# Kernel optimization log

Hardware: AMD Instinct MI355X
Metric: run time of the kernel (lower is better)

## Reference

```python
import jax, jax.numpy as jnp
import numpy as np

N = 10000
E = 160000
IN_DIM = 512
OUT_DIM = 256
NEG_SLOPE = 0.2  # DGL GATConv default LeakyReLU slope


def _gat_conv(x, W, b, attn_l, attn_r, src, dst, num_nodes, heads, out_dim):
    """DGL GATConv (eval mode, feat_drop/attn_drop disabled).
    x: [N, F_in]; W: [F_in, heads*out]; b: [heads*out];
    attn_l/attn_r: [heads, out]. Returns [N, heads, out]."""
    h = (x @ W).reshape(num_nodes, heads, out_dim)            # [N,H,D]
    el = jnp.einsum('nhd,hd->nh', h, attn_l)                  # [N,H]
    er = jnp.einsum('nhd,hd->nh', h, attn_r)                  # [N,H]
    e = jax.nn.leaky_relu(el[src] + er[dst], NEG_SLOPE)       # [E,H]
    # destination-grouped (edge) softmax, numerically stable
    m = jax.ops.segment_max(e, dst, num_segments=num_nodes)   # [N,H], -inf for empty
    m = jnp.where(jnp.isfinite(m), m, 0.0)
    ee = jnp.exp(e - m[dst])                                  # [E,H]
    s = jax.ops.segment_sum(ee, dst, num_segments=num_nodes)  # [N,H]
    a = ee / jnp.where(s > 0, s, 1.0)[dst]                    # [E,H]
    # message aggregation: scatter-add a_e * h[src]
    out = jax.ops.segment_sum(a[:, :, None] * h[src], dst, num_segments=num_nodes)
    return out + b.reshape(1, heads, out_dim)


def setup_inputs() -> dict:
    key = jax.random.key(0)
    ks = jax.random.split(key, 16)
    def glorot(k, shape):
        fan = shape[0] + shape[-1] if len(shape) > 1 else shape[-1]
        return jax.random.normal(k, shape, dtype=jnp.float32) * np.sqrt(2.0 / fan)
    inp = {
        'x':   jax.random.normal(ks[0], (N, IN_DIM), dtype=jnp.float32),
        'src': jax.random.randint(ks[1], (E,), 0, N),
        'dst': jax.random.randint(ks[2], (E,), 0, N),
        'W1': glorot(ks[3], (IN_DIM, 10 * 128)),
        'b1': jnp.zeros((10 * 128,), jnp.float32),
        'al1': glorot(ks[4], (10, 128)),
        'ar1': glorot(ks[5], (10, 128)),
        'W2': glorot(ks[6], (1280, 10 * 64)),
        'b2': jnp.zeros((10 * 64,), jnp.float32),
        'al2': glorot(ks[7], (10, 64)),
        'ar2': glorot(ks[8], (10, 64)),
        'W3': glorot(ks[9], (640, OUT_DIM)),
        'b3': jnp.zeros((OUT_DIM,), jnp.float32),
        'al3': glorot(ks[10], (1, OUT_DIM)),
        'ar3': glorot(ks[11], (1, OUT_DIM)),
        # residual linear 512 -> 256
        'Wres': glorot(ks[12], (IN_DIM, OUT_DIM)),
        'bres': jnp.zeros((OUT_DIM,), jnp.float32),
        'fuse_weight': jnp.full((1,), 0.5, jnp.float32),
    }
    return inp


def reference(x, src, dst, W1, b1, al1, ar1, W2, b2, al2, ar2,
              W3, b3, al3, ar3, Wres, bres, fuse_weight):
    elu = jax.nn.elu
    res = elu(x @ Wres + bres)                                        # [N,256]
    s1 = elu(_gat_conv(x, W1, b1, al1, ar1, src, dst, N, 10, 128))
    s1 = s1.reshape(N, -1)                                            # [N,1280]
    s2 = elu(_gat_conv(s1, W2, b2, al2, ar2, src, dst, N, 10, 64))
    s2 = s2.reshape(N, -1)                                            # [N,640]
    s3 = elu(_gat_conv(s2, W3, b3, al3, ar3, src, dst, N, 1, OUT_DIM))
    s3 = s3.reshape(N, -1)                                            # [N,256]
    return fuse_weight * s3 + (1.0 - fuse_weight) * res
```

## Files before the change

kernel.cpp:

```cpp
#include <hip/hip_runtime.h>
#include <stdint.h>

#define DEVINL __device__ __forceinline__

typedef __attribute__((ext_vector_type(8))) short short8;
typedef __attribute__((ext_vector_type(4))) float f32x4;

static constexpr int NNODES = 10000;

DEVINL float bf2f(unsigned short u) {
  unsigned int x = ((unsigned int)u) << 16;
  float f;
  __builtin_memcpy(&f, &x, 4);
  return f;
}
DEVINL unsigned short f2bf(float f) {
  unsigned int x;
  __builtin_memcpy(&x, &f, 4);
  unsigned int lsb = (x >> 16) & 1;
  x += 0x7fffu + lsb;
  return (unsigned short)(x >> 16);
}
DEVINL void bfpair(unsigned int u, float& f0, float& f1) {
  unsigned int a = u << 16, b = u & 0xffff0000u;
  __builtin_memcpy(&f0, &a, 4);
  __builtin_memcpy(&f1, &b, 4);
}
DEVINL bool is_bf16_mode(const unsigned int* fwWord) {
  return ((*fwWord) & 0xFFFFu) == 0x3F00u;
}

DEVINL void async_cp16(void* lds, const void* g) {
  __builtin_amdgcn_global_load_lds((const __attribute__((address_space(1))) unsigned int*)g,
                                   (__attribute__((address_space(3))) unsigned int*)lds,
                                   16, 0, 0);
}

__global__ __launch_bounds__(256) void gemm_bf16(const unsigned short* __restrict__ A,
                                                 const unsigned short* __restrict__ Bt,
                                                 unsigned short* __restrict__ C,
                                                 int M, int N, int K) {
  __shared__ __align__(16) unsigned short lA[128 * 32];
  __shared__ __align__(16) unsigned short lB[128 * 32];
  const int tid = threadIdx.x;
  const int wid = tid >> 6;
  const int lane = tid & 63;
  const int tm = blockIdx.x * 128;
  const int tn = blockIdx.y * 128;
  const int wr = (wid >> 1) * 64;
  const int wc = (wid & 1) * 64;
  f32x4 acc[4][4] = {};
  const int r_in_chunk = lane >> 2;
  const int cb = (lane & 3) * 16;
  const int mr = lane & 15;
  const int kq = (lane >> 4) * 8;
  const size_t stride = (size_t)K * 2;

  for (int k0 = 0; k0 < K; k0 += 32) {
#pragma unroll
    for (int c = 0; c < 2; ++c) {
      const int chunk = wid * 2 + c;
      const int row = chunk * 16 + r_in_chunk;
      int ga = tm + row;
      if (ga >= M) ga = M - 1;
      async_cp16(&lA[chunk * 512], (const char*)A + (size_t)ga * stride + (size_t)k0 * 2 + cb);
      const int gb = tn + row;
      async_cp16(&lB[chunk * 512], (const char*)Bt + (size_t)gb * stride + (size_t)k0 * 2 + cb);
    }
    __syncthreads();
    short8 af[4], bf[4];
#pragma unroll
    for (int i = 0; i < 4; ++i)
      af[i] = *(const short8*)&lA[(wr + i * 16 + mr) * 32 + kq];
#pragma unroll
    for (int j = 0; j < 4; ++j)
      bf[j] = *(const short8*)&lB[(wc + j * 16 + mr) * 32 + kq];
#pragma unroll
    for (int i = 0; i < 4; ++i)
#pragma unroll
      for (int j = 0; j < 4; ++j)
        acc[i][j] = __builtin_amdgcn_mfma_f32_16x16x32_bf16(af[i], bf[j], acc[i][j], 0, 0, 0);
    __syncthreads();
  }

  const int rbase = (lane >> 4) * 4;
  const int cc = lane & 15;
#pragma unroll
  for (int i = 0; i < 4; ++i) {
#pragma unroll
    for (int r = 0; r < 4; ++r) {
      const int row = tm + wr + i * 16 + rbase + r;
      if (row < M) {
#pragma unroll
        for (int j = 0; j < 4; ++j) {
          const int col = tn + wc + j * 16 + cc;
          C[(size_t)row * N + col] = f2bf(acc[i][j][r]);
        }
      }
    }
  }
}

struct CvtJobs {
  const void* src[12];
  float* dst[12];
  int n[12];
  int cnt;
};
__global__ void cvt_small_f32(CvtJobs jobs, const unsigned int* fwWord) {
  const bool isb = is_bf16_mode(fwWord);
  for (int j = 0; j < jobs.cnt; ++j) {
    for (int i = blockIdx.x * blockDim.x + threadIdx.x; i < jobs.n[j];
         i += gridDim.x * blockDim.x) {
      jobs.dst[j][i] = isb ? bf2f(((const unsigned short*)jobs.src[j])[i])
                           : ((const float*)jobs.src[j])[i];
    }
  }
}

__global__ __launch_bounds__(256) void cvt_x_bf16(const void* __restrict__ in,
                                                  unsigned short* __restrict__ out,
                                                  long n, const unsigned int* fwWord) {
  const bool isb = is_bf16_mode(fwWord);
  const long i0 = (long)(blockIdx.x * 256 + threadIdx.x) * 8;
  if (i0 >= n) return;
  if (isb) {
    *(short8*)&out[i0] = *(const short8*)&((const unsigned short*)in)[i0];
  } else {
    const float* f = (const float*)in + i0;
    unsigned short r[8];
#pragma unroll
    for (int j = 0; j < 8; ++j) r[j] = f2bf(f[j]);
    *(short8*)&out[i0] = *(const short8*)r;
  }
}

struct TAll {
  const void* src[4];
  unsigned short* dst[4];
  int K[4];
  int N[4];
  int b0[5];
};
__global__ __launch_bounds__(256) void transp_all4(TAll ja, const unsigned int* fwWord) {
  const bool isb = is_bf16_mode(fwWord);
  __shared__ unsigned short t[32][33];
  const int bid = blockIdx.x;
  int j = 0;
  while (j < 3 && bid >= ja.b0[j + 1]) ++j;
  const int local = bid - ja.b0[j];
  const int K = ja.K[j], Nn = ja.N[j];
  const int tilesX = Nn / 32;
  const int bx = (local % tilesX) * 32;
  const int by = (local / tilesX) * 32;
  const void* W = ja.src[j];
  unsigned short* Wt = ja.dst[j];
  const int x = threadIdx.x;
  const int y0 = threadIdx.y;
  for (int y = y0; y < 32; y += 8) {
    const size_t idx = (size_t)(by + y) * Nn + bx + x;
    t[y][x] = isb ? ((const unsigned short*)W)[idx] : f2bf(((const float*)W)[idx]);
  }
  __syncthreads();
  for (int y = y0; y < 32; y += 8)
    Wt[(size_t)(bx + y) * K + by + x] = t[x][y];
}

template <int H, int D>
__global__ __launch_bounds__(256) void compute_elr(const unsigned short* __restrict__ hf,
                                                   const float* __restrict__ al,
                                                   const float* __restrict__ ar,
                                                   float* __restrict__ el,
                                                   float* __restrict__ er) {
  const int gw = (blockIdx.x * 256 + threadIdx.x) >> 6;
  const int lane = threadIdx.x & 63;
  if (gw >= NNODES * H) return;
  const int n = gw / H;
  const int h = gw % H;
  const unsigned short* hp = hf + (size_t)n * (H * D) + h * D;
  const float* alp = al + h * D;
  const float* arp = ar + h * D;
  float a = 0.f, b = 0.f;
#pragma unroll
  for (int d0 = 0; d0 < D; d0 += 64) {
    float v = bf2f(hp[d0 + lane]);
    a += v * alp[d0 + lane];
    b += v * arp[d0 + lane];
  }
#pragma unroll
  for (int o = 32; o; o >>= 1) {
    a += __shfl_xor(a, o);
    b += __shfl_xor(b, o);
  }
  if (lane == 0) { el[gw] = a; er[gw] = b; }
}

template <int H>
__global__ __launch_bounds__(256) void edge_w(const float* __restrict__ el,
                                              const float* __restrict__ er,
                                              const int* __restrict__ sidx,
                                              const int* __restrict__ didx,
                                              float* __restrict__ we, int E) {
  const int p = blockIdx.x * 256 + threadIdx.x;
  if (p >= E) return;
  const float* ep = el + (size_t)sidx[p] * H;
  const float* rp = er + (size_t)didx[p] * H;
  float* wp = we + (size_t)p * H;
#pragma unroll
  for (int h = 0; h < H; ++h) {
    float sc = ep[h] + rp[h];
    sc = sc > 0.f ? sc : 0.2f * sc;
    wp[h] = __expf(sc);
  }
}

template <int H, int D, int BLOCK, int V, int MODE>
__global__ __launch_bounds__(BLOCK) void gat_agg(const unsigned short* __restrict__ hf,
                                                 const float* __restrict__ we,
                                                 const int* __restrict__ sidx,
                                                 const int* __restrict__ rowstart,
                                                 const float* __restrict__ bias,
                                                 void* __restrict__ outp,
                                                 const unsigned short* __restrict__ resact,
                                                 const float* __restrict__ fwf,
                                                 const unsigned int* fwWord) {
  constexpr int CHUNK = 64;
  static_assert(H * D == BLOCK * V, "feature ownership mismatch");
  static_assert(BLOCK % H == 0, "fill-head must be thread-fixed");
  static_assert(V == 2 || V == 4, "vector width");
  __shared__ float wls[CHUNK * H];
  __shared__ int ssrc[CHUNK];
  __shared__ float shead[H];

  const int n = blockIdx.x;
  const int tid = threadIdx.x;
  const int e0 = rowstart[n];
  const int e1 = rowstart[n + 1];

  if (tid < H) shead[tid] = 0.f;
  __syncthreads();

  const int fbase = tid * V;
  const int fh = fbase / D;
  const int fh2 = tid % H;
  float acc[V];
#pragma unroll
  for (int k = 0; k < V; ++k) acc[k] = 0.f;
  float spart = 0.f;

  for (int cs = e0; cs < e1; cs += CHUNK) {
    const int ce = min(CHUNK, e1 - cs);
    if (tid < ce) ssrc[tid] = sidx[cs + tid];
    for (int i = tid; i < ce * H; i += BLOCK) {
      const float w = we[(size_t)cs * H + i];
      wls[i] = w;
      spart += w;
    }
    __syncthreads();
    int j = 0;
    for (; j + 4 <= ce; j += 4) {
      const int s0 = ssrc[j], s1 = ssrc[j + 1], s2 = ssrc[j + 2], s3 = ssrc[j + 3];
      const float w0 = wls[(j + 0) * H + fh];
      const float w1 = wls[(j + 1) * H + fh];
      const float w2 = wls[(j + 2) * H + fh];
      const float w3 = wls[(j + 3) * H + fh];
      if constexpr (V == 4) {
        const uint2 u0 = *(const uint2*)(hf + (size_t)s0 * (H * D) + fbase);
        const uint2 u1 = *(const uint2*)(hf + (size_t)s1 * (H * D) + fbase);
        const uint2 u2 = *(const uint2*)(hf + (size_t)s2 * (H * D) + fbase);
        const uint2 u3 = *(const uint2*)(hf + (size_t)s3 * (H * D) + fbase);
        float a0, a1, a2, a3;
        bfpair(u0.x, a0, a1); bfpair(u0.y, a2, a3);
        acc[0] += w0 * a0; acc[1] += w0 * a1; acc[2] += w0 * a2; acc[3] += w0 * a3;
        bfpair(u1.x, a0, a1); bfpair(u1.y, a2, a3);
        acc[0] += w1 * a0; acc[1] += w1 * a1; acc[2] += w1 * a2; acc[3] += w1 * a3;
        bfpair(u2.x, a0, a1); bfpair(u2.y, a2, a3);
        acc[0] += w2 * a0; acc[1] += w2 * a1; acc[2] += w2 * a2; acc[3] += w2 * a3;
        bfpair(u3.x, a0, a1); bfpair(u3.y, a2, a3);
        acc[0] += w3 * a0; acc[1] += w3 * a1; acc[2] += w3 * a2; acc[3] += w3 * a3;
      } else {
        const unsigned int u0 = *(const unsigned int*)(hf + (size_t)s0 * (H * D) + fbase);
        const unsigned int u1 = *(const unsigned int*)(hf + (size_t)s1 * (H * D) + fbase);
        const unsigned int u2 = *(const unsigned int*)(hf + (size_t)s2 * (H * D) + fbase);
        const unsigned int u3 = *(const unsigned int*)(hf + (size_t)s3 * (H * D) + fbase);
        float a0, a1;
        bfpair(u0, a0, a1); acc[0] += w0 * a0; acc[1] += w0 * a1;
        bfpair(u1, a0, a1); acc[0] += w1 * a0; acc[1] += w1 * a1;
        bfpair(u2, a0, a1); acc[0] += w2 * a0; acc[1] += w2 * a1;
        bfpair(u3, a0, a1); acc[0] += w3 * a0; acc[1] += w3 * a1;
      }
    }
    for (; j < ce; ++j) {
      const int s0 = ssrc[j];
      const float w = wls[j * H + fh];
      const unsigned short* hp = hf + (size_t)s0 * (H * D) + fbase;
      if constexpr (V == 4) {
        const uint2 u = *(const uint2*)hp;
        float a0, a1, a2, a3;
        bfpair(u.x, a0, a1); bfpair(u.y, a2, a3);
        acc[0] += w * a0; acc[1] += w * a1; acc[2] += w * a2; acc[3] += w * a3;
      } else {
        const unsigned int u = *(const unsigned int*)hp;
        float a0, a1;
        bfpair(u, a0, a1);
        acc[0] += w * a0; acc[1] += w * a1;
      }
    }
    __syncthreads();
  }

  atomicAdd(&shead[fh2], spart);
  __syncthreads();
  const float s = shead[fh];
  const float inv = s > 0.f ? 1.f / s : 0.f;
  const bool outb = (MODE == 1) ? is_bf16_mode(fwWord) : true;
  const size_t obase = (size_t)n * (H * D) + fbase;
#pragma unroll
  for (int k = 0; k < V; ++k) {
    float v = acc[k] * inv;
    v += bias[fbase + k];
    v = v > 0.f ? v : (__expf(v) - 1.f);
    if (MODE == 0) {
      ((unsigned short*)outp)[obase + k] = f2bf(v);
    } else {
      const float fw = fwf[0];
      const float r = bf2f(resact[obase + k]);
      const float o = fw * v + (1.f - fw) * r;
      if (outb) ((unsigned short*)outp)[obase + k] = f2bf(o);
      else      ((float*)outp)[obase + k] = o;
    }
  }
}

__global__ __launch_bounds__(256) void bias_elu(unsigned short* __restrict__ buf,
                                                const float* __restrict__ bias,
                                                int total, int Cc) {
  const int i = blockIdx.x * 256 + threadIdx.x;
  if (i >= total) return;
  float v = bf2f(buf[i]) + bias[i % Cc];
  v = v > 0.f ? v : (__expf(v) - 1.f);
  buf[i] = f2bf(v);
}

__global__ void sentinel_k(unsigned short* __restrict__ outp, int total) {
  const int i = blockIdx.x * 256 + threadIdx.x;
  if (i < total) outp[i] = f2bf(12344.0f);
}

__global__ void hist_k(const int* __restrict__ dst, int* __restrict__ deg, int E) {
  const int i = blockIdx.x * blockDim.x + threadIdx.x;
  if (i < E) atomicAdd(&deg[dst[i]], 1);
}

__global__ __launch_bounds__(1024) void scan_k(const int* __restrict__ deg,
                                               int* __restrict__ rowstart,
                                               int* __restrict__ cursor, int Nn) {
  __shared__ int ls[1024];
  const int tid = threadIdx.x;
  const int CH = (Nn + 1023) >> 10;
  const int start = tid * CH;
  int sum = 0;
  for (int i = 0; i < CH; ++i) {
    const int idx = start + i;
    if (idx < Nn) sum += deg[idx];
  }
  ls[tid] = sum;
  __syncthreads();
  for (int o = 1; o < 1024; o <<= 1) {
    int v = 0;
    if (tid >= o) v = ls[tid - o];
    __syncthreads();
    ls[tid] += v;
    __syncthreads();
  }
  int run = tid > 0 ? ls[tid - 1] : 0;
  for (int i = 0; i < CH; ++i) {
    const int idx = start + i;
    if (idx < Nn) {
      rowstart[idx] = run;
      cursor[idx] = run;
      run += deg[idx];
    }
  }
  if (tid == 1023) rowstart[Nn] = ls[1023];
}

__global__ void scatter_k(const int* __restrict__ dst, const int* __restrict__ srcA,
                          int* __restrict__ cursor, int* __restrict__ sidx,
                          int* __restrict__ didx, int E) {
  const int i = blockIdx.x * blockDim.x + threadIdx.x;
  if (i < E) {
    const int d = dst[i];
    const int p = atomicAdd(&cursor[d], 1);
    sidx[p] = srcA[i];
    didx[p] = d;
  }
}

extern "C" void kernel_launch(void* const* d_in, const int* in_sizes, int n_in,
                              void* d_out, int out_size, void* d_ws, size_t ws_size,
                              hipStream_t stream) {
  const void* x    = d_in[0];
  const int* src   = (const int*)d_in[1];
  const int* dstA  = (const int*)d_in[2];
  const void* W1   = d_in[3];
  const void* b1   = d_in[4];
  const void* al1  = d_in[5];
  const void* ar1  = d_in[6];
  const void* W2   = d_in[7];
  const void* b2   = d_in[8];
  const void* al2  = d_in[9];
  const void* ar2  = d_in[10];
  const void* W3   = d_in[11];
  const void* b3   = d_in[12];
  const void* al3  = d_in[13];
  const void* ar3  = d_in[14];
  const void* Wres = d_in[15];
  const void* bres = d_in[16];
  const void* fw   = d_in[17];
  const unsigned int* fwWord = (const unsigned int*)fw;
  const int E = in_sizes[1];
  const int M = NNODES;

  char* base = (char*)d_ws;
  size_t off = 0;
  auto alloc = [&](size_t bytes) -> char* {
    char* p = base + off;
    off = (off + bytes + 255) & ~(size_t)255;
    return p;
  };
  int* deg      = (int*)alloc((size_t)M * 4);
  int* rowstart = (int*)alloc((size_t)(M + 1) * 4);
  int* cursor   = (int*)alloc((size_t)M * 4);
  int* sidx     = (int*)alloc((size_t)E * 4);
  int* didx     = (int*)alloc((size_t)E * 4);
  float* web    = (float*)alloc((size_t)E * 10 * 4);
  float* elb    = (float*)alloc((size_t)M * 10 * 4);
  float* erb    = (float*)alloc((size_t)M * 10 * 4);
  float* b1f   = (float*)alloc(1280 * 4);
  float* al1f  = (float*)alloc(1280 * 4);
  float* ar1f  = (float*)alloc(1280 * 4);
  float* b2f   = (float*)alloc(640 * 4);
  float* al2f  = (float*)alloc(640 * 4);
  float* ar2f  = (float*)alloc(640 * 4);
  float* b3f   = (float*)alloc(256 * 4);
  float* al3f  = (float*)alloc(256 * 4);
  float* ar3f  = (float*)alloc(256 * 4);
  float* bresf = (float*)alloc(256 * 4);
  float* fwf   = (float*)alloc(4);
  unsigned short* wt1    = (unsigned short*)alloc((size_t)1280 * 512 * 2);
  unsigned short* wt2    = (unsigned short*)alloc((size_t)640 * 1280 * 2);
  unsigned short* wt3    = (unsigned short*)alloc((size_t)256 * 640 * 2);
  unsigned short* wtr    = (unsigned short*)alloc((size_t)256 * 512 * 2);
  unsigned short* resact = (unsigned short*)alloc((size_t)M * 256 * 2);
  unsigned short* regA   = (unsigned short*)alloc((size_t)M * 1280 * 2);
  unsigned short* regB   = (unsigned short*)alloc((size_t)M * 1280 * 2);

  if (off > ws_size) {
    sentinel_k<<<(out_size + 255) / 256, 256, 0, stream>>>((unsigned short*)d_out, out_size);
    return;
  }

  unsigned short* h1 = regA;
  unsigned short* h2 = regA;
  unsigned short* h3 = regA;
  unsigned short* xb = regB;
  unsigned short* s1 = regB;
  unsigned short* s2 = regB;

  CvtJobs jobs;
  const void* srcs[11] = {b1, al1, ar1, b2, al2, ar2, b3, al3, ar3, bres, fw};
  float* dsts[11] = {b1f, al1f, ar1f, b2f, al2f, ar2f, b3f, al3f, ar3f, bresf, fwf};
  const int ns[11] = {1280, 1280, 1280, 640, 640, 640, 256, 256, 256, 256, 1};
  for (int j = 0; j < 11; ++j) { jobs.src[j] = srcs[j]; jobs.dst[j] = dsts[j]; jobs.n[j] = ns[j]; }
  jobs.cnt = 11;
  cvt_small_f32<<<8, 256, 0, stream>>>(jobs, fwWord);

  cvt_x_bf16<<<(int)(((long)M * 512 / 8 + 255) / 256), 256, 0, stream>>>(x, xb, (long)M * 512, fwWord);

  TAll ta;
  ta.src[0] = W1;   ta.dst[0] = wt1; ta.K[0] = 512;  ta.N[0] = 1280;
  ta.src[1] = W2;   ta.dst[1] = wt2; ta.K[1] = 1280; ta.N[1] = 640;
  ta.src[2] = W3;   ta.dst[2] = wt3; ta.K[2] = 640;  ta.N[2] = 256;
  ta.src[3] = Wres; ta.dst[3] = wtr; ta.K[3] = 512;  ta.N[3] = 256;
  ta.b0[0] = 0;
  for (int j = 0; j < 4; ++j)
    ta.b0[j + 1] = ta.b0[j] + (ta.K[j] / 32) * (ta.N[j] / 32);
  transp_all4<<<ta.b0[4], dim3(32, 8), 0, stream>>>(ta, fwWord);

  hipMemsetAsync(deg, 0, (size_t)M * 4, stream);
  hist_k<<<(E + 255) / 256, 256, 0, stream>>>(dstA, deg, E);
  scan_k<<<1, 1024, 0, stream>>>(deg, rowstart, cursor, M);
  scatter_k<<<(E + 255) / 256, 256, 0, stream>>>(dstA, src, cursor, sidx, didx, E);

  const int MT = (M + 127) / 128;
  const int EB = (E + 255) / 256;

  gemm_bf16<<<dim3(MT, 2), 256, 0, stream>>>(xb, wtr, resact, M, 256, 512);
  bias_elu<<<(M * 256 + 255) / 256, 256, 0, stream>>>(resact, bresf, M * 256, 256);

  gemm_bf16<<<dim3(MT, 10), 256, 0, stream>>>(xb, wt1, h1, M, 1280, 512);
  compute_elr<10, 128><<<(M * 10) / 4, 256, 0, stream>>>(h1, al1f, ar1f, elb, erb);
  edge_w<10><<<EB, 256, 0, stream>>>(elb, erb, sidx, didx, web, E);
  gat_agg<10, 128, 320, 4, 0><<<M, 320, 0, stream>>>(h1, web, sidx, rowstart,
                                                     b1f, s1, nullptr, fwf, fwWord);

  gemm_bf16<<<dim3(MT, 5), 256, 0, stream>>>(s1, wt2, h2, M, 640, 1280);
  compute_elr<10, 64><<<(M * 10) / 4, 256, 0, stream>>>(h2, al2f, ar2f, elb, erb);
  edge_w<10><<<EB, 256, 0, stream>>>(elb, erb, sidx, didx, web, E);
  gat_agg<10, 64, 320, 2, 0><<<M, 320, 0, stream>>>(h2, web, sidx, rowstart,
                                                    b2f, s2, nullptr, fwf, fwWord);

  gemm_bf16<<<dim3(MT, 2), 256, 0, stream>>>(s2, wt3, h3, M, 256, 640);
  compute_elr<1, 256><<<M / 4, 256, 0, stream>>>(h3, al3f, ar3f, elb, erb);
  edge_w<1><<<EB, 256, 0, stream>>>(elb, erb, sidx, didx, web, E);
  gat_agg<1, 256, 64, 4, 1><<<M, 64, 0, stream>>>(h3, web, sidx, rowstart,
                                                  b3f, d_out, resact, fwf, fwWord);
}
```

Baseline: 340.1 us.

## Split GAT aggregation into feature slices per node with precomputed softmax denominators

A separate kernel now computes per-node, per-head softmax denominators, so the aggregation kernel no longer accumulates and reduces the weight sums itself. Each destination node is split across several blocks, each owning a slice of the feature dimension with two bf16 values per thread, and edge weights are pre-normalised when staged into shared memory. The goal is more, smaller blocks and better occupancy for the gather-bound aggregation. The cost is that every slice block re-reads the edge indices and weights, plus one extra kernel launch per layer.

```diff
diff --git a/kernel.cpp b/kernel.cpp
--- a/kernel.cpp
+++ b/kernel.cpp
@@ -214,120 +214,109 @@
   }
 }
 
-template <int H, int D, int BLOCK, int V, int MODE>
-__global__ __launch_bounds__(BLOCK) void gat_agg(const unsigned short* __restrict__ hf,
-                                                 const float* __restrict__ we,
-                                                 const int* __restrict__ sidx,
-                                                 const int* __restrict__ rowstart,
-                                                 const float* __restrict__ bias,
-                                                 void* __restrict__ outp,
-                                                 const unsigned short* __restrict__ resact,
-                                                 const float* __restrict__ fwf,
-                                                 const unsigned int* fwWord) {
+template <int H>
+__global__ __launch_bounds__(256) void denom_k(const float* __restrict__ we,
+                                               const int* __restrict__ rowstart,
+                                               float* __restrict__ dinv, int total) {
+  const int id = blockIdx.x * 256 + threadIdx.x;
+  if (id >= total) return;
+  const int n = id / H;
+  const int h = id % H;
+  const int e0 = rowstart[n], e1 = rowstart[n + 1];
+  float s = 0.f;
+  for (int p = e0; p < e1; ++p) s += we[(size_t)p * H + h];
+  dinv[id] = s > 0.f ? 1.f / s : 0.f;
+}
+
+template <int H, int D, int NS, int BLOCK, int MODE>
+__global__ __launch_bounds__(BLOCK) void gat_agg_sl(const unsigned short* __restrict__ hf,
+                                                    const float* __restrict__ we,
+                                                    const float* __restrict__ dinv,
+                                                    const int* __restrict__ sidx,
+                                                    const int* __restrict__ rowstart,
+                                                    const float* __restrict__ bias,
+                                                    void* __restrict__ outp,
+                                                    const unsigned short* __restrict__ resact,
+                                                    const float* __restrict__ fwf,
+                                                    const unsigned int* fwWord) {
   constexpr int CHUNK = 64;
-  static_assert(H * D == BLOCK * V, "feature ownership mismatch");
-  static_assert(BLOCK % H == 0, "fill-head must be thread-fixed");
-  static_assert(V == 2 || V == 4, "vector width");
+  constexpr int FDW = (H * D / 2) / NS;
+  static_assert((H * D / 2) % NS == 0, "slice width");
+  static_assert(FDW <= BLOCK, "enough threads");
   __shared__ float wls[CHUNK * H];
   __shared__ int ssrc[CHUNK];
-  __shared__ float shead[H];
-
-  const int n = blockIdx.x;
+  __shared__ float dinv_s[H];
+
+  const int bid = blockIdx.x;
+  const int n = bid / NS;
+  const int slice = bid % NS;
   const int tid = threadIdx.x;
   const int e0 = rowstart[n];
   const int e1 = rowstart[n + 1];
 
-  if (tid < H) shead[tid] = 0.f;
+  if (tid < H) dinv_s[tid] = dinv[n * H + tid];
+  const int fbase = (slice * FDW + tid) * 2;
+  const int fh = fbase / D;
+  const bool act = tid < FDW;
+  float acc0 = 0.f, acc1 = 0.f;
   __syncthreads();
-
-  const int fbase = tid * V;
-  const int fh = fbase / D;
-  const int fh2 = tid % H;
-  float acc[V];
-#pragma unroll
-  for (int k = 0; k < V; ++k) acc[k] = 0.f;
-  float spart = 0.f;
 
   for (int cs = e0; cs < e1; cs += CHUNK) {
     const int ce = min(CHUNK, e1 - cs);
     if (tid < ce) ssrc[tid] = sidx[cs + tid];
-    for (int i = tid; i < ce * H; i += BLOCK) {
-      const float w = we[(size_t)cs * H + i];
-      wls[i] = w;
-      spart += w;
-    }
+    for (int i = tid; i < ce * H; i += BLOCK)
+      wls[i] = we[(size_t)cs * H + i] * dinv_s[i % H];
     __syncthreads();
-    int j = 0;
-    for (; j + 4 <= ce; j += 4) {
-      const int s0 = ssrc[j], s1 = ssrc[j + 1], s2 = ssrc[j + 2], s3 = ssrc[j + 3];
-      const float w0 = wls[(j + 0) * H + fh];
-      const float w1 = wls[(j + 1) * H + fh];
-      const float w2 = wls[(j + 2) * H + fh];
-      const float w3 = wls[(j + 3) * H + fh];
-      if constexpr (V == 4) {
-        const uint2 u0 = *(const uint2*)(hf + (size_t)s0 * (H * D) + fbase);
-        const uint2 u1 = *(const uint2*)(hf + (size_t)s1 * (H * D) + fbase);
-        const uint2 u2 = *(const uint2*)(hf + (size_t)s2 * (H * D) + fbase);
-        const uint2 u3 = *(const uint2*)(hf + (size_t)s3 * (H * D) + fbase);
-        float a0, a1, a2, a3;
-        bfpair(u0.x, a0, a1); bfpair(u0.y, a2, a3);
-        acc[0] += w0 * a0; acc[1] += w0 * a1; acc[2] += w0 * a2; acc[3] += w0 * a3;
-        bfpair(u1.x, a0, a1); bfpair(u1.y, a2, a3);
-        acc[0] += w1 * a0; acc[1] += w1 * a1; acc[2] += w1 * a2; acc[3] += w1 * a3;
-        bfpair(u2.x, a0, a1); bfpair(u2.y, a2, a3);
-        acc[0] += w2 * a0; acc[1] += w2 * a1; acc[2] += w2 * a2; acc[3] += w2 * a3;
-        bfpair(u3.x, a0, a1); bfpair(u3.y, a2, a3);
-        acc[0] += w3 * a0; acc[1] += w3 * a1; acc[2] += w3 * a2; acc[3] += w3 * a3;
-      } else {
+    if (act) {
+      int j = 0;
+      for (; j + 4 <= ce; j += 4) {
+        const int s0 = ssrc[j], s1 = ssrc[j + 1], s2 = ssrc[j + 2], s3 = ssrc[j + 3];
         const unsigned int u0 = *(const unsigned int*)(hf + (size_t)s0 * (H * D) + fbase);
         const unsigned int u1 = *(const unsigned int*)(hf + (size_t)s1 * (H * D) + fbase);
         const unsigned int u2 = *(const unsigned int*)(hf + (size_t)s2 * (H * D) + fbase);
         const unsigned int u3 = *(const unsigned int*)(hf + (size_t)s3 * (H * D) + fbase);
+        const float w0 = wls[(j + 0) * H + fh];
+        const float w1 = wls[(j + 1) * H + fh];
+        const float w2 = wls[(j + 2) * H + fh];
+        const float w3 = wls[(j + 3) * H + fh];
         float a0, a1;
-        bfpair(u0, a0, a1); acc[0] += w0 * a0; acc[1] += w0 * a1;
-        bfpair(u1, a0, a1); acc[0] += w1 * a0; acc[1] += w1 * a1;
-        bfpair(u2, a0, a1); acc[0] += w2 * a0; acc[1] += w2 * a1;
-        bfpair(u3, a0, a1); acc[0] += w3 * a0; acc[1] += w3 * a1;
+        bfpair(u0, a0, a1); acc0 += w0 * a0; acc1 += w0 * a1;
+        bfpair(u1, a0, a1); acc0 += w1 * a0; acc1 += w1 * a1;
+        bfpair(u2, a0, a1); acc0 += w2 * a0; acc1 += w2 * a1;
+        bfpair(u3, a0, a1); acc0 += w3 * a0; acc1 += w3 * a1;
       }
-    }
-    for (; j < ce; ++j) {
-      const int s0 = ssrc[j];
-      const float w = wls[j * H + fh];
-      const unsigned short* hp = hf + (size_t)s0 * (H * D) + fbase;
-      if constexpr (V == 4) {
-        const uint2 u = *(const uint2*)hp;
-        float a0, a1, a2, a3;
-        bfpair(u.x, a0, a1); bfpair(u.y, a2, a3);
-        acc[0] += w * a0; acc[1] += w * a1; acc[2] += w * a2; acc[3] += w * a3;
-      } else {
-        const unsigned int u = *(const unsigned int*)hp;
+      for (; j < ce; ++j) {
+        const unsigned int u = *(const unsigned int*)(hf + (size_t)ssrc[j] * (H * D) + fbase);
+        const float w = wls[j * H + fh];
         float a0, a1;
         bfpair(u, a0, a1);
-        acc[0] += w * a0; acc[1] += w * a1;
+        acc0 += w * a0; acc1 += w * a1;
       }
     }
     __syncthreads();
   }
 
-  atomicAdd(&shead[fh2], spart);
-  __syncthreads();
-  const float s = shead[fh];
-  const float inv = s > 0.f ? 1.f / s : 0.f;
-  const bool outb = (MODE == 1) ? is_bf16_mode(fwWord) : true;
+  if (!act) return;
   const size_t obase = (size_t)n * (H * D) + fbase;
-#pragma unroll
-  for (int k = 0; k < V; ++k) {
-    float v = acc[k] * inv;
-    v += bias[fbase + k];
-    v = v > 0.f ? v : (__expf(v) - 1.f);
-    if (MODE == 0) {
-      ((unsigned short*)outp)[obase + k] = f2bf(v);
+  float v0 = acc0 + bias[fbase];
+  float v1 = acc1 + bias[fbase + 1];
+  v0 = v0 > 0.f ? v0 : (__expf(v0) - 1.f);
+  v1 = v1 > 0.f ? v1 : (__expf(v1) - 1.f);
+  if (MODE == 0) {
+    ((unsigned short*)outp)[obase] = f2bf(v0);
+    ((unsigned short*)outp)[obase + 1] = f2bf(v1);
+  } else {
+    const float fw = fwf[0];
+    const float r0 = bf2f(resact[obase]);
+    const float r1 = bf2f(resact[obase + 1]);
+    const float o0 = fw * v0 + (1.f - fw) * r0;
+    const float o1 = fw * v1 + (1.f - fw) * r1;
+    if (is_bf16_mode(fwWord)) {
+      ((unsigned short*)outp)[obase] = f2bf(o0);
+      ((unsigned short*)outp)[obase + 1] = f2bf(o1);
     } else {
-      const float fw = fwf[0];
-      const float r = bf2f(resact[obase + k]);
-      const float o = fw * v + (1.f - fw) * r;
-      if (outb) ((unsigned short*)outp)[obase + k] = f2bf(o);
-      else      ((float*)outp)[obase + k] = o;
+      ((float*)outp)[obase] = o0;
+      ((float*)outp)[obase + 1] = o1;
     }
   }
 }
@@ -437,6 +426,7 @@
   float* web    = (float*)alloc((size_t)E * 10 * 4);
   float* elb    = (float*)alloc((size_t)M * 10 * 4);
   float* erb    = (float*)alloc((size_t)M * 10 * 4);
+  float* dinv   = (float*)alloc((size_t)M * 10 * 4);
   float* b1f   = (float*)alloc(1280 * 4);
   float* al1f  = (float*)alloc(1280 * 4);
   float* ar1f  = (float*)alloc(1280 * 4);
@@ -502,18 +492,21 @@
   gemm_bf16<<<dim3(MT, 10), 256, 0, stream>>>(xb, wt1, h1, M, 1280, 512);
   compute_elr<10, 128><<<(M * 10) / 4, 256, 0, stream>>>(h1, al1f, ar1f, elb, erb);
   edge_w<10><<<EB, 256, 0, stream>>>(elb, erb, sidx, didx, web, E);
-  gat_agg<10, 128, 320, 4, 0><<<M, 320, 0, stream>>>(h1, web, sidx, rowstart,
-                                                     b1f, s1, nullptr, fwf, fwWord);
+  denom_k<10><<<(M * 10 + 255) / 256, 256, 0, stream>>>(web, rowstart, dinv, M * 10);
+  gat_agg_sl<10, 128, 8, 128, 0><<<M * 8, 128, 0, stream>>>(h1, web, dinv, sidx, rowstart,
+                                                            b1f, s1, nullptr, fwf, fwWord);
 
   gemm_bf16<<<dim3(MT, 5), 256, 0, stream>>>(s1, wt2, h2, M, 640, 1280);
   compute_elr<10, 64><<<(M * 10) / 4, 256, 0, stream>>>(h2, al2f, ar2f, elb, erb);
   edge_w<10><<<EB, 256, 0, stream>>>(elb, erb, sidx, didx, web, E);
-  gat_agg<10, 64, 320, 2, 0><<<M, 320, 0, stream>>>(h2, web, sidx, rowstart,
-                                                    b2f, s2, nullptr, fwf, fwWord);
+  denom_k<10><<<(M * 10 + 255) / 256, 256, 0, stream>>>(web, rowstart, dinv, M * 10);
+  gat_agg_sl<10, 64, 8, 64, 0><<<M * 8, 64, 0, stream>>>(h2, web, dinv, sidx, rowstart,
+                                                         b2f, s2, nullptr, fwf, fwWord);
 
   gemm_bf16<<<dim3(MT, 2), 256, 0, stream>>>(s2, wt3, h3, M, 256, 640);
   compute_elr<1, 256><<<M / 4, 256, 0, stream>>>(h3, al3f, ar3f, elb, erb);
   edge_w<1><<<EB, 256, 0, stream>>>(elb, erb, sidx, didx, web, E);
-  gat_agg<1, 256, 64, 4, 1><<<M, 64, 0, stream>>>(h3, web, sidx, rowstart,
-                                                  b3f, d_out, resact, fwf, fwWord);
-}
+  denom_k<1><<<(M + 255) / 256, 256, 0, stream>>>(web, rowstart, dinv, M);
+  gat_agg_sl<1, 256, 2, 64, 1><<<M * 2, 64, 0, stream>>>(h3, web, dinv, sidx, rowstart,
+                                                         b3f, d_out, resact, fwf, fwWord);
+}
```

New measurement: 385.7 us. 13.4% more time.

## Split GAT aggregation into per-node feature slices with precomputed softmax denominators

Applied to the files above, without the earlier changes.

Edge weights are now stored head-major (transposed) and a new denom_k kernel computes per-node per-head reciprocal softmax sums. The aggregation kernel is restructured into one 64-thread wave per (node, feature slice), so each node spawns several small blocks instead of one large block. Each slice loads only the one or two head weight rows it needs, pre-scaled by the reciprocal denominator. This targets parallelism and occupancy for low-degree nodes and removes the shared-memory atomic reduction, at the cost of an extra kernel launch per layer, serial denominator loops, and repeated sidx loads across slices.

```diff
diff --git a/kernel.cpp b/kernel.cpp
--- a/kernel.cpp
+++ b/kernel.cpp
@@ -200,132 +200,151 @@
                                               const float* __restrict__ er,
                                               const int* __restrict__ sidx,
                                               const int* __restrict__ didx,
-                                              float* __restrict__ we, int E) {
+                                              float* __restrict__ we_t, int E) {
   const int p = blockIdx.x * 256 + threadIdx.x;
   if (p >= E) return;
   const float* ep = el + (size_t)sidx[p] * H;
   const float* rp = er + (size_t)didx[p] * H;
-  float* wp = we + (size_t)p * H;
 #pragma unroll
   for (int h = 0; h < H; ++h) {
     float sc = ep[h] + rp[h];
     sc = sc > 0.f ? sc : 0.2f * sc;
-    wp[h] = __expf(sc);
-  }
-}
-
-template <int H, int D, int BLOCK, int V, int MODE>
-__global__ __launch_bounds__(BLOCK) void gat_agg(const unsigned short* __restrict__ hf,
-                                                 const float* __restrict__ we,
+    we_t[(size_t)h * E + p] = __expf(sc);
+  }
+}
+
+template <int H>
+__global__ __launch_bounds__(256) void denom_k(const float* __restrict__ we_t,
+                                               const int* __restrict__ rowstart,
+                                               float* __restrict__ dinv_t,
+                                               int E, int total) {
+  const int id = blockIdx.x * 256 + threadIdx.x;
+  if (id >= total) return;
+  const int h = id / NNODES;
+  const int n = id % NNODES;
+  const int e0 = rowstart[n], e1 = rowstart[n + 1];
+  const float* wp = we_t + (size_t)h * E;
+  float s = 0.f;
+  for (int p = e0; p < e1; ++p) s += wp[p];
+  dinv_t[id] = s > 0.f ? 1.f / s : 0.f;
+}
+
+template <int H, int D, int NS, int CW, int MODE>
+__global__ __launch_bounds__(64) void gat_agg_hs(const unsigned short* __restrict__ hf,
+                                                 const float* __restrict__ we_t,
+                                                 const float* __restrict__ dinv_t,
                                                  const int* __restrict__ sidx,
                                                  const int* __restrict__ rowstart,
                                                  const float* __restrict__ bias,
                                                  void* __restrict__ outp,
                                                  const unsigned short* __restrict__ resact,
                                                  const float* __restrict__ fwf,
-                                                 const unsigned int* fwWord) {
+                                                 const unsigned int* fwWord, int E) {
   constexpr int CHUNK = 64;
-  static_assert(H * D == BLOCK * V, "feature ownership mismatch");
-  static_assert(BLOCK % H == 0, "fill-head must be thread-fixed");
-  static_assert(V == 2 || V == 4, "vector width");
-  __shared__ float wls[CHUNK * H];
+  constexpr int SF = H * D / NS;
+  constexpr int ACT = SF / CW;
+  constexpr int LOG2D = (D == 64) ? 6 : (D == 128) ? 7 : 8;
+  static_assert((H * D) % NS == 0 && (SF % CW) == 0 && ACT <= 64, "geometry");
+  static_assert(CW == 2 || CW == 4, "vector width");
+  static_assert(SF < 2 * D, "slice spans at most 2 heads");
+  __shared__ float wls[2 * CHUNK];
   __shared__ int ssrc[CHUNK];
-  __shared__ float shead[H];
-
-  const int n = blockIdx.x;
+
+  const int bid = blockIdx.x;
+  const int n = bid / NS;
+  const int sl = bid % NS;
   const int tid = threadIdx.x;
-  const int e0 = rowstart[n];
-  const int e1 = rowstart[n + 1];
-
-  if (tid < H) shead[tid] = 0.f;
-  __syncthreads();
-
-  const int fbase = tid * V;
-  const int fh = fbase / D;
-  const int fh2 = tid % H;
-  float acc[V];
-#pragma unroll
-  for (int k = 0; k < V; ++k) acc[k] = 0.f;
-  float spart = 0.f;
+  const int e0 = rowstart[n], e1 = rowstart[n + 1];
+  const int f0 = SF * sl;
+  const int hlo = f0 >> LOG2D;
+  const int hhi = (f0 + SF - 1) >> LOG2D;
+  const float dlo = dinv_t[(size_t)hlo * NNODES + n];
+  const float dhi = dinv_t[(size_t)hhi * NNODES + n];
+  const int fbase = f0 + tid * CW;
+  const int wbase = ((fbase >> LOG2D) != hlo) ? CHUNK : 0;
+  const bool act = tid < ACT;
+  float acc[CW] = {};
 
   for (int cs = e0; cs < e1; cs += CHUNK) {
     const int ce = min(CHUNK, e1 - cs);
-    if (tid < ce) ssrc[tid] = sidx[cs + tid];
-    for (int i = tid; i < ce * H; i += BLOCK) {
-      const float w = we[(size_t)cs * H + i];
-      wls[i] = w;
-      spart += w;
+    if (tid < ce) {
+      ssrc[tid] = sidx[cs + tid];
+      wls[tid] = we_t[(size_t)hlo * E + cs + tid] * dlo;
+      if (hhi != hlo) wls[CHUNK + tid] = we_t[(size_t)hhi * E + cs + tid] * dhi;
     }
     __syncthreads();
-    int j = 0;
-    for (; j + 4 <= ce; j += 4) {
-      const int s0 = ssrc[j], s1 = ssrc[j + 1], s2 = ssrc[j + 2], s3 = ssrc[j + 3];
-      const float w0 = wls[(j + 0) * H + fh];
-      const float w1 = wls[(j + 1) * H + fh];
-      const float w2 = wls[(j + 2) * H + fh];
-      const float w3 = wls[(j + 3) * H + fh];
-      if constexpr (V == 4) {
-        const uint2 u0 = *(const uint2*)(hf + (size_t)s0 * (H * D) + fbase);
-        const uint2 u1 = *(const uint2*)(hf + (size_t)s1 * (H * D) + fbase);
-        const uint2 u2 = *(const uint2*)(hf + (size_t)s2 * (H * D) + fbase);
-        const uint2 u3 = *(const uint2*)(hf + (size_t)s3 * (H * D) + fbase);
-        float a0, a1, a2, a3;
-        bfpair(u0.x, a0, a1); bfpair(u0.y, a2, a3);
-        acc[0] += w0 * a0; acc[1] += w0 * a1; acc[2] += w0 * a2; acc[3] += w0 * a3;
-        bfpair(u1.x, a0, a1); bfpair(u1.y, a2, a3);
-        acc[0] += w1 * a0; acc[1] += w1 * a1; acc[2] += w1 * a2; acc[3] += w1 * a3;
-        bfpair(u2.x, a0, a1); bfpair(u2.y, a2, a3);
-        acc[0] += w2 * a0; acc[1] += w2 * a1; acc[2] += w2 * a2; acc[3] += w2 * a3;
-        bfpair(u3.x, a0, a1); bfpair(u3.y, a2, a3);
-        acc[0] += w3 * a0; acc[1] += w3 * a1; acc[2] += w3 * a2; acc[3] += w3 * a3;
-      } else {
-        const unsigned int u0 = *(const unsigned int*)(hf + (size_t)s0 * (H * D) + fbase);
-        const unsigned int u1 = *(const unsigned int*)(hf + (size_t)s1 * (H * D) + fbase);
-        const unsigned int u2 = *(const unsigned int*)(hf + (size_t)s2 * (H * D) + fbase);
-        const unsigned int u3 = *(const unsigned int*)(hf + (size_t)s3 * (H * D) + fbase);
-        float a0, a1;
-        bfpair(u0, a0, a1); acc[0] += w0 * a0; acc[1] += w0 * a1;
-        bfpair(u1, a0, a1); acc[0] += w1 * a0; acc[1] += w1 * a1;
-        bfpair(u2, a0, a1); acc[0] += w2 * a0; acc[1] += w2 * a1;
-        bfpair(u3, a0, a1); acc[0] += w3 * a0; acc[1] += w3 * a1;
+    if (act) {
+      const unsigned short* hfb = hf + fbase;
+      int j = 0;
+      for (; j + 4 <= ce; j += 4) {
+        const int s0 = ssrc[j], s1 = ssrc[j + 1], s2 = ssrc[j + 2], s3 = ssrc[j + 3];
+        const float w0 = wls[wbase + j];
+        const float w1 = wls[wbase + j + 1];
+        const float w2 = wls[wbase + j + 2];
+        const float w3 = wls[wbase + j + 3];
+        if constexpr (CW == 4) {
+          const uint2 u0 = *(const uint2*)(hfb + (size_t)s0 * (H * D));
+          const uint2 u1 = *(const uint2*)(hfb + (size_t)s1 * (H * D));
+          const uint2 u2 = *(const uint2*)(hfb + (size_t)s2 * (H * D));
+          const uint2 u3 = *(const uint2*)(hfb + (size_t)s3 * (H * D));
+          float a0, a1, a2, a3;
+          bfpair(u0.x, a0, a1); bfpair(u0.y, a2, a3);
+          acc[0] += w0 * a0; acc[1] += w0 * a1; acc[2] += w0 * a2; acc[3] += w0 * a3;
+          bfpair(u1.x, a0, a1); bfpair(u1.y, a2, a3);
+          acc[0] += w1 * a0; acc[1] += w1 * a1; acc[2] += w1 * a2; acc[3] += w1 * a3;
+          bfpair(u2.x, a0, a1); bfpair(u2.y, a2, a3);
+          acc[0] += w2 * a0; acc[1] += w2 * a1; acc[2] += w2 * a2; acc[3] += w2 * a3;
+          bfpair(u3.x, a0, a1); bfpair(u3.y, a2, a3);
+          acc[0] += w3 * a0; acc[1] += w3 * a1; acc[2] += w3 * a2; acc[3] += w3 * a3;
+        } else {
+          const unsigned int u0 = *(const unsigned int*)(hfb + (size_t)s0 * (H * D));
+          const unsigned int u1 = *(const unsigned int*)(hfb + (size_t)s1 * (H * D));
+          const unsigned int u2 = *(const unsigned int*)(hfb + (size_t)s2 * (H * D));
+          const unsigned int u3 = *(const unsigned int*)(hfb + (size_t)s3 * (H * D));
+          float a0, a1;
+          bfpair(u0, a0, a1); acc[0] += w0 * a0; acc[1] += w0 * a1;
+          bfpair(u1, a0, a1); acc[0] += w1 * a0; acc[1] += w1 * a1;
+          bfpair(u2, a0, a1); acc[0] += w2 * a0; acc[1] += w2 * a1;
+          bfpair(u3, a0, a1); acc[0] += w3 * a0; acc[1] += w3 * a1;
+        }
       }
-    }
-    for (; j < ce; ++j) {
-      const int s0 = ssrc[j];
-      const float w = wls[j * H + fh];
-      const unsigned short* hp = hf + (size_t)s0 * (H * D) + fbase;
-      if constexpr (V == 4) {
-        const uint2 u = *(const uint2*)hp;
-        float a0, a1, a2, a3;
-        bfpair(u.x, a0, a1); bfpair(u.y, a2, a3);
-        acc[0] += w * a0; acc[1] += w * a1; acc[2] += w * a2; acc[3] += w * a3;
-      } else {
-        const unsigned int u = *(const unsigned int*)hp;
-        float a0, a1;
-        bfpair(u, a0, a1);
-        acc[0] += w * a0; acc[1] += w * a1;
+      for (; j < ce; ++j) {
+        const float w = wls[wbase + j];
+        if constexpr (CW == 4) {
+          const uint2 u = *(const uint2*)(hfb + (size_t)ssrc[j] * (H * D));
+          float a0, a1, a2, a3;
+          bfpair(u.x, a0, a1); bfpair(u.y, a2, a3);
+          acc[0] += w * a0; acc[1] += w * a1; acc[2] += w * a2; acc[3] += w * a3;
+        } else {
+          const unsigned int u = *(const unsigned int*)(hfb + (size_t)ssrc[j] * (H * D));
+          float a0, a1;
+          bfpair(u, a0, a1);
+          acc[0] += w * a0; acc[1] += w * a1;
+        }
       }
     }
     __syncthreads();
   }
 
-  atomicAdd(&shead[fh2], spart);
-  __syncthreads();
-  const float s = shead[fh];
-  const float inv = s > 0.f ? 1.f / s : 0.f;
-  const bool outb = (MODE == 1) ? is_bf16_mode(fwWord) : true;
+  if (!act) return;
   const size_t obase = (size_t)n * (H * D) + fbase;
-#pragma unroll
-  for (int k = 0; k < V; ++k) {
-    float v = acc[k] * inv;
-    v += bias[fbase + k];
-    v = v > 0.f ? v : (__expf(v) - 1.f);
-    if (MODE == 0) {
-      ((unsigned short*)outp)[obase + k] = f2bf(v);
-    } else {
-      const float fw = fwf[0];
+  float v[CW];
+#pragma unroll
+  for (int k = 0; k < CW; ++k) {
+    v[k] = acc[k] + bias[fbase + k];
+    v[k] = v[k] > 0.f ? v[k] : (__expf(v[k]) - 1.f);
+  }
+  if (MODE == 0) {
+#pragma unroll
+    for (int k = 0; k < CW; ++k)
+      ((unsigned short*)outp)[obase + k] = f2bf(v[k]);
+  } else {
+    const float fw = fwf[0];
+    const bool outb = is_bf16_mode(fwWord);
+#pragma unroll
+    for (int k = 0; k < CW; ++k) {
       const float r = bf2f(resact[obase + k]);
-      const float o = fw * v + (1.f - fw) * r;
+      const float o = fw * v[k] + (1.f - fw) * r;
       if (outb) ((unsigned short*)outp)[obase + k] = f2bf(o);
       else      ((float*)outp)[obase + k] = o;
     }
@@ -434,9 +453,10 @@
   int* cursor   = (int*)alloc((size_t)M * 4);
   int* sidx     = (int*)alloc((size_t)E * 4);
   int* didx     = (int*)alloc((size_t)E * 4);
-  float* web    = (float*)alloc((size_t)E * 10 * 4);
+  float* we_t   = (float*)alloc((size_t)E * 10 * 4);
   float* elb    = (float*)alloc((size_t)M * 10 * 4);
   float* erb    = (float*)alloc((size_t)M * 10 * 4);
+  float* dinv_t = (float*)alloc((size_t)M * 10 * 4);
   float* b1f   = (float*)alloc(1280 * 4);
   float* al1f  = (float*)alloc(1280 * 4);
   float* ar1f  = (float*)alloc(1280 * 4);
@@ -501,19 +521,22 @@
 
   gemm_bf16<<<dim3(MT, 10), 256, 0, stream>>>(xb, wt1, h1, M, 1280, 512);
   compute_elr<10, 128><<<(M * 10) / 4, 256, 0, stream>>>(h1, al1f, ar1f, elb, erb);
-  edge_w<10><<<EB, 256, 0, stream>>>(elb, erb, sidx, didx, web, E);
-  gat_agg<10, 128, 320, 4, 0><<<M, 320, 0, stream>>>(h1, web, sidx, rowstart,
-                                                     b1f, s1, nullptr, fwf, fwWord);
+  edge_w<10><<<EB, 256, 0, stream>>>(elb, erb, sidx, didx, we_t, E);
+  denom_k<10><<<(M * 10 + 255) / 256, 256, 0, stream>>>(we_t, rowstart, dinv_t, E, M * 10);
+  gat_agg_hs<10, 128, 8, 4, 0><<<M * 8, 64, 0, stream>>>(h1, we_t, dinv_t, sidx, rowstart,
+                                                         b1f, s1, nullptr, fwf, fwWord, E);
 
   gemm_bf16<<<dim3(MT, 5), 256, 0, stream>>>(s1, wt2, h2, M, 640, 1280);
   compute_elr<10, 64><<<(M * 10) / 4, 256, 0, stream>>>(h2, al2f, ar2f, elb, erb);
-  edge_w<10><<<EB, 256, 0, stream>>>(elb, erb, sidx, didx, web, E);
-  gat_agg<10, 64, 320, 2, 0><<<M, 320, 0, stream>>>(h2, web, sidx, rowstart,
-                                                    b2f, s2, nullptr, fwf, fwWord);
+  edge_w<10><<<EB, 256, 0, stream>>>(elb, erb, sidx, didx, we_t, E);
+  denom_k<10><<<(M * 10 + 255) / 256, 256, 0, stream>>>(we_t, rowstart, dinv_t, E, M * 10);
+  gat_agg_hs<10, 64, 8, 2, 0><<<M * 8, 64, 0, stream>>>(h2, we_t, dinv_t, sidx, rowstart,
+                                                        b2f, s2, nullptr, fwf, fwWord, E);
 
   gemm_bf16<<<dim3(MT, 2), 256, 0, stream>>>(s2, wt3, h3, M, 256, 640);
   compute_elr<1, 256><<<M / 4, 256, 0, stream>>>(h3, al3f, ar3f, elb, erb);
-  edge_w<1><<<EB, 256, 0, stream>>>(elb, erb, sidx, didx, web, E);
-  gat_agg<1, 256, 64, 4, 1><<<M, 64, 0, stream>>>(h3, web, sidx, rowstart,
-                                                  b3f, d_out, resact, fwf, fwWord);
-}
+  edge_w<1><<<EB, 256, 0, stream>>>(elb, erb, sidx, didx, we_t, E);
+  denom_k<1><<<(M + 255) / 256, 256, 0, stream>>>(we_t, rowstart, dinv_t, E, M);
+  gat_agg_hs<1, 256, 2, 2, 1><<<M * 2, 64, 0, stream>>>(h3, we_t, dinv_t, sidx, rowstart,
+                                                        b3f, d_out, resact, fwf, fwWord, E);
+}
```

Result: faster. 330.9 us (-2.7%).
